# Performance work log

Hardware: AMD Instinct MI355X
Metric: run time of the kernel (lower is better)

The kernel has to match this reference:

```python
import jax, jax.numpy as jnp
import numpy as np

D = 512      # d_model
S = 8        # num_quantum_states
B, T = 16, 1024
LN_EPS = 1e-5


def setup_inputs() -> dict:
    key = jax.random.key(0)
    ks = jax.random.split(key, 10)
    sc = lambda fan_in: 1.0 / np.sqrt(fan_in)
    return {
        "x": jax.random.normal(ks[0], (B, T, D), dtype=jnp.float32),
        # entanglement gates: torch Linear weight [out=D, in=2D], bias [D], stacked over S
        "W_ent": jax.random.uniform(ks[1], (S, D, 2 * D), minval=-sc(2 * D), maxval=sc(2 * D)),
        "b_ent": jax.random.uniform(ks[2], (S, D), minval=-sc(2 * D), maxval=sc(2 * D)),
        # measurement MLP: Linear(D*S->D), LayerNorm(D), Tanh, Linear(D->1)
        "m1_w": jax.random.uniform(ks[3], (D, D * S), minval=-sc(D * S), maxval=sc(D * S)),
        "m1_b": jax.random.uniform(ks[4], (D,), minval=-sc(D * S), maxval=sc(D * S)),
        "ln_g": jnp.ones((D,), dtype=jnp.float32),
        "ln_b": jnp.zeros((D,), dtype=jnp.float32),
        "m2_w": jax.random.uniform(ks[5], (1, D), minval=-sc(D), maxval=sc(D)),
        "m2_b": jax.random.uniform(ks[6], (1,), minval=-sc(D), maxval=sc(D)),
    }


def _layernorm(h, g, b):
    mu = jnp.mean(h, axis=-1, keepdims=True)
    var = jnp.mean(jnp.square(h - mu), axis=-1, keepdims=True)
    return (h - mu) * jax.lax.rsqrt(var + LN_EPS) * g + b


def reference(x, W_ent, b_ent, m1_w, m1_b, ln_g, ln_b, m2_w, m2_b):
    b_, t_, d_ = x.shape
    s_ = W_ent.shape[0]
    # gate(cat[x_i, x_j]).mean(dim=2) == x_i @ W1^T + mean_j(x_j) @ W2^T + b  (exact algebra)
    W1 = W_ent[:, :, :d_]   # [S, D, D] acts on x_i
    W2 = W_ent[:, :, d_:]   # [S, D, D] acts on x_j (mean over j)
    xbar = jnp.mean(x, axis=1)                                   # [B, D]
    ent = (jnp.einsum('btd,sed->bste', x, W1)                    # [B, S, T, D]
           + jnp.einsum('bd,sed->bse', xbar, W2)[:, :, None, :]
           + b_ent[None, :, None, :])
    # permute(0,2,3,1).reshape(B,T,D*S): feature layout is (d, s) fastest on s
    qv = jnp.transpose(ent, (0, 2, 3, 1)).reshape(b_, t_, d_ * s_)
    h = jnp.tanh(_layernorm(qv @ m1_w.T + m1_b, ln_g, ln_b))     # [B, T, D]
    attn_logits = h @ m2_w.T + m2_b                              # [B, T, 1]
    attn_weights = jax.nn.softmax(attn_logits, axis=1)
    context = jnp.sum(attn_weights * x, axis=1)                  # [B, D]
    return context, attn_weights
```

## Files before the change

kernel.cpp:

```cpp
#include <hip/hip_runtime.h>
#include <hip/hip_bf16.h>

typedef __attribute__((ext_vector_type(8))) short bf16x8;
typedef __attribute__((ext_vector_type(4))) float f32x4;

__device__ __forceinline__ float bf2f(unsigned short u) {
    union { unsigned int i; float f; } c; c.i = ((unsigned int)u) << 16; return c.f;
}
__device__ __forceinline__ unsigned short f2bf(float f) {
    union { float f; unsigned int i; } c; c.f = f;
    unsigned int x = c.i;
    x += 0x7fffu + ((x >> 16) & 1u);
    return (unsigned short)(x >> 16);
}
__device__ __forceinline__ float tanh_fast(float v) {
    float a = fabsf(v);
    a = fminf(a, 15.0f);
    float e = __expf(2.0f * a);
    float t = 1.0f - 2.0f / (e + 1.0f);
    return copysignf(t, v);
}

#define GLOAD_LDS16(gp, lp) \
    __builtin_amdgcn_global_load_lds((const __attribute__((address_space(1))) void*)(gp), \
                                     (__attribute__((address_space(3))) void*)(lp), 16, 0, 0)

#define MFMA(a, b, c) __builtin_amdgcn_mfma_f32_16x16x32_bf16((a), (b), (c), 0, 0, 0)

#define SBAR()  __builtin_amdgcn_s_barrier()
#define SCHED0() __builtin_amdgcn_sched_barrier(0)


__global__ void k_sumx(const float* __restrict__ x, float* __restrict__ sumx) {
    int b = blockIdx.x, tc = blockIdx.y;
    int tid = threadIdx.x;
    const float* xp = x + ((size_t)b * 1024 + tc * 64) * 512;
    float a0 = 0.f, a1 = 0.f;
    for (int t = 0; t < 64; ++t) {
        a0 += xp[(size_t)t * 512 + tid];
        a1 += xp[(size_t)t * 512 + tid + 256];
    }
    atomicAdd(&sumx[b * 512 + tid], a0);
    atomicAdd(&sumx[b * 512 + tid + 256], a1);
}

__global__ void k_prepA(const float* __restrict__ m1w, const float* __restrict__ bent,
                        unsigned short* __restrict__ Abf, float* __restrict__ bias2) {
    int i = blockIdx.x, tid = threadIdx.x;
    const float* row = m1w + (size_t)i * 4096;
    float acc = 0.f;
    #pragma unroll
    for (int q = 0; q < 4; ++q) {
        int col = q * 1024 + tid * 4;
        float4 v = *(const float4*)(row + col);
        ushort4 o;
        o.x = f2bf(v.x); o.y = f2bf(v.y); o.z = f2bf(v.z); o.w = f2bf(v.w);
        *(ushort4*)(Abf + (size_t)i * 4096 + col) = o;
        int e0 = col >> 3, s0 = col & 7;
        acc += v.x * bent[(s0    ) * 512 + e0];
        acc += v.y * bent[(s0 + 1) * 512 + e0];
        acc += v.z * bent[(s0 + 2) * 512 + e0];
        acc += v.w * bent[(s0 + 3) * 512 + e0];
    }
    #pragma unroll
    for (int off = 32; off; off >>= 1) acc += __shfl_xor(acc, off);
    __shared__ float r4[4];
    if ((tid & 63) == 0) r4[tid >> 6] = acc;
    __syncthreads();
    if (tid == 0) bias2[i] = r4[0] + r4[1] + r4[2] + r4[3];
}

__global__ void k_conv_W(const float* __restrict__ W, unsigned short* __restrict__ WT) {
    __shared__ float tile[128][33];
    int e0 = blockIdx.x * 16;
    int j0 = blockIdx.y * 32;
    int tid = threadIdx.x;
    int tx = tid & 31, ty = tid >> 5;
    #pragma unroll
    for (int q = 0; q < 16; ++q) {
        int lk = q * 8 + ty;
        int de = lk >> 3, s = lk & 7;
        int r = s * 512 + e0 + de;
        tile[lk][tx] = W[(size_t)r * 1024 + j0 + tx];
    }
    __syncthreads();
    int j = tid >> 3, ck = (tid & 7) * 16;
    unsigned short* dst = WT + (size_t)(j0 + j) * 4096 + e0 * 8 + ck;
    #pragma unroll
    for (int g = 0; g < 4; ++g) {
        ushort4 o;
        o.x = f2bf(tile[ck + g * 4 + 0][j]);
        o.y = f2bf(tile[ck + g * 4 + 1][j]);
        o.z = f2bf(tile[ck + g * 4 + 2][j]);
        o.w = f2bf(tile[ck + g * 4 + 3][j]);
        *(ushort4*)(dst + g * 4) = o;
    }
}

__launch_bounds__(512, 2)
__global__ void k_gemm1(const unsigned short* __restrict__ Abf,
                        const unsigned short* __restrict__ WT,
                        float* __restrict__ CpL, float* __restrict__ CpR) {
    __shared__ __align__(16) unsigned short sA[2][64 * 64];
    __shared__ __align__(16) unsigned short sB[2][256 * 64];
    int i0 = blockIdx.x * 64;
    int j0 = blockIdx.y * 256;
    int kbase = blockIdx.z * 512;
    int tid = threadIdx.x, lane = tid & 63, w = tid >> 6;
    int wm = w >> 2, wn = w & 3;
    int lr = lane >> 3, sl = lane & 7;
    int lo = lane & 15, hi = lane >> 4;
    int arow = w * 8 + lr;
    const unsigned short* gA = Abf + (size_t)(i0 + arow) * 4096 + kbase + ((sl ^ lr) << 3);
    const unsigned short* gB0 = WT + (size_t)(j0 + w * 32 + 0 * 8 + lr) * 4096 + kbase + ((sl ^ lr) << 3);
    const unsigned short* gB1 = WT + (size_t)(j0 + w * 32 + 1 * 8 + lr) * 4096 + kbase + ((sl ^ lr) << 3);
    const unsigned short* gB2 = WT + (size_t)(j0 + w * 32 + 2 * 8 + lr) * 4096 + kbase + ((sl ^ lr) << 3);
    const unsigned short* gB3 = WT + (size_t)(j0 + w * 32 + 3 * 8 + lr) * 4096 + kbase + ((sl ^ lr) << 3);
    bool left = (blockIdx.y < 2);
    f32x4 acc[2][4] = {};

#define G1_STAGE(tt, bufn)                                                    \
    do {                                                                      \
        int koff = (tt) * 64;                                                 \
        GLOAD_LDS16(gA + koff, &sA[bufn][w * 8 * 64]);                        \
        GLOAD_LDS16(gB0 + koff, &sB[bufn][(w * 32 + 0) * 64]);                \
        GLOAD_LDS16(gB1 + koff, &sB[bufn][(w * 32 + 8) * 64]);                \
        GLOAD_LDS16(gB2 + koff, &sB[bufn][(w * 32 + 16) * 64]);               \
        GLOAD_LDS16(gB3 + koff, &sB[bufn][(w * 32 + 24) * 64]);               \
        SCHED0();                                                             \
    } while (0)

    G1_STAGE(0, 0);
    #pragma unroll
    for (int t = 0; t < 8; ++t) {
        int buf = t & 1;
        if (t < 7) {
            G1_STAGE(t + 1, buf ^ 1);
            asm volatile("s_waitcnt vmcnt(5)" ::: "memory");
        } else {
            asm volatile("s_waitcnt vmcnt(0)" ::: "memory");
        }
        SCHED0(); SBAR(); SCHED0();
        __builtin_amdgcn_s_setprio(1);
        #pragma unroll
        for (int kk = 0; kk < 2; ++kk) {
            int slotX = ((kk * 4 + hi) ^ (lo & 7)) << 3;
            bf16x8 a0 = *(const bf16x8*)(&sA[buf][(wm * 32 +      lo) * 64 + slotX]);
            bf16x8 a1 = *(const bf16x8*)(&sA[buf][(wm * 32 + 16 + lo) * 64 + slotX]);
            #pragma unroll
            for (int n = 0; n < 4; ++n) {
                bf16x8 bb = *(const bf16x8*)(&sB[buf][(wn * 64 + n * 16 + lo) * 64 + slotX]);
                if (left) {
                    acc[0][n] = MFMA(a0, bb, acc[0][n]);
                    acc[1][n] = MFMA(a1, bb, acc[1][n]);
                } else {
                    acc[0][n] = MFMA(bb, a0, acc[0][n]);
                    acc[1][n] = MFMA(bb, a1, acc[1][n]);
                }
            }
        }
        __builtin_amdgcn_s_setprio(0);
        if (t < 7) { SCHED0(); SBAR(); SCHED0(); }
    }
#undef G1_STAGE

    int ksoff = blockIdx.z * 262144;
    if (left) {
        #pragma unroll
        for (int m = 0; m < 2; ++m) {
            int ib = i0 + wm * 32 + m * 16 + hi * 4;
            #pragma unroll
            for (int n = 0; n < 4; ++n) {
                int j = j0 + wn * 64 + n * 16 + lo;
                #pragma unroll
                for (int r = 0; r < 4; ++r)
                    CpL[ksoff + (ib + r) * 512 + j] = acc[m][n][r];
            }
        }
    } else {
        #pragma unroll
        for (int m = 0; m < 2; ++m) {
            int ic = i0 + wm * 32 + m * 16 + lo;
            #pragma unroll
            for (int n = 0; n < 4; ++n) {
                int db = j0 - 512 + wn * 64 + n * 16 + hi * 4;
                #pragma unroll
                for (int r = 0; r < 4; ++r)
                    CpR[ksoff + (db + r) * 512 + ic] = acc[m][n][r];
            }
        }
    }
}

__global__ void k_reduce(const float* __restrict__ CpL, const float* __restrict__ CpR,
                         unsigned short* __restrict__ M1bf, unsigned short* __restrict__ M2t) {
    int bx = blockIdx.x;
    const float* Cp = (bx < 256) ? CpL : CpR;
    unsigned short* ob = (bx < 256) ? M1bf : M2t;
    int gid = (bx & 255) * 256 + threadIdx.x;
    float4 s = ((const float4*)Cp)[gid];
    #pragma unroll
    for (int ks = 1; ks < 8; ++ks) {
        float4 t = ((const float4*)Cp)[ks * 65536 + gid];
        s.x += t.x; s.y += t.y; s.z += t.z; s.w += t.w;
    }
    ushort4 o;
    o.x = f2bf(s.x); o.y = f2bf(s.y); o.z = f2bf(s.z); o.w = f2bf(s.w);
    ((ushort4*)ob)[gid] = o;
}

__global__ void k_cb(const float* __restrict__ sumx, const unsigned short* __restrict__ M2t,
                     const float* __restrict__ bias2, const float* __restrict__ m1b,
                     float* __restrict__ cbo) {
    int b = blockIdx.x, i0 = blockIdx.y * 64;
    int tid = threadIdx.x;
    int il = tid & 63, dq = tid >> 6;
    const float* sx = sumx + b * 512 + dq * 128;
    const unsigned short* mp = M2t + (size_t)dq * 128 * 512 + i0 + il;
    float acc = 0.f;
    #pragma unroll 4
    for (int dd = 0; dd < 128; ++dd)
        acc += sx[dd] * bf2f(mp[(size_t)dd * 512]);
    __shared__ float sPart[4][64];
    sPart[dq][il] = acc;
    __syncthreads();
    if (tid < 64) {
        float v = sPart[0][tid] + sPart[1][tid] + sPart[2][tid] + sPart[3][tid];
        cbo[b * 512 + i0 + tid] = v * (1.0f / 1024.0f) + bias2[i0 + tid] + m1b[i0 + tid];
    }
}

__launch_bounds__(512)
__global__ void k_gemm2(const float* __restrict__ x,
                        const unsigned short* __restrict__ M1bf,
                        const float* __restrict__ cb,
                        const float* __restrict__ lng, const float* __restrict__ lnb,
                        const float* __restrict__ m2w, const float* __restrict__ m2b,
                        float* __restrict__ logits) {
    __shared__ __align__(16) unsigned short sA[2][64 * 64];
    __shared__ __align__(16) unsigned short sB[2][512 * 64];
    __shared__ float sRed[2][8][64];
    __shared__ float sMu[64], sRs[64];
    __shared__ float sLp[8][64];
    int bt0 = blockIdx.x * 64;
    int b = bt0 >> 10;
    int tid = threadIdx.x, lane = tid & 63, w = tid >> 6;
    int wm = w >> 2, wn = w & 3;
    int lo = lane & 15, hi = lane >> 4;
    int lr = lane >> 3, sl = lane & 7;
    int arow = tid >> 3, aslot = tid & 7;
    const float* gA = x + (size_t)(bt0 + arow) * 512 + aslot * 8;
    int aoff = arow * 64 + ((aslot ^ (arow & 7)) << 3);
    const unsigned short* gB[8];
    #pragma unroll
    for (int g = 0; g < 8; ++g)
        gB[g] = M1bf + (size_t)(w * 64 + g * 8 + lr) * 512 + ((sl ^ lr) << 3);
    float4 pf0, pf1;
    f32x4 acc[2][8] = {};

#define G2_ISSUE(tt, bufn)                                                    \
    do {                                                                      \
        pf0 = *(const float4*)(gA + (tt) * 64);                               \
        pf1 = *(const float4*)(gA + (tt) * 64 + 4);                           \
        SCHED0();                                                             \
        _Pragma("unroll")                                                     \
        for (int g = 0; g < 8; ++g)                                           \
            GLOAD_LDS16(gB[g] + (tt) * 64, &sB[bufn][(w * 64 + g * 8) * 64]); \
        SCHED0();                                                             \
    } while (0)

#define G2_AWRITE(bufn)                                                      \
    do {                                                                     \
        bf16x8 pk;                                                           \
        pk[0] = (short)f2bf(pf0.x); pk[1] = (short)f2bf(pf0.y);              \
        pk[2] = (short)f2bf(pf0.z); pk[3] = (short)f2bf(pf0.w);              \
        pk[4] = (short)f2bf(pf1.x); pk[5] = (short)f2bf(pf1.y);              \
        pk[6] = (short)f2bf(pf1.z); pk[7] = (short)f2bf(pf1.w);              \
        *(bf16x8*)(&sA[bufn][aoff]) = pk;                                    \
    } while (0)

    G2_ISSUE(0, 0);
    asm volatile("s_waitcnt vmcnt(8)" ::: "memory");
    SCHED0();
    G2_AWRITE(0);
    asm volatile("s_waitcnt lgkmcnt(0)" ::: "memory");
    SCHED0();

    #pragma unroll
    for (int t = 0; t < 8; ++t) {
        int buf = t & 1;
        if (t < 7) {
            G2_ISSUE(t + 1, buf ^ 1);
            asm volatile("s_waitcnt vmcnt(10)" ::: "memory");
        } else {
            asm volatile("s_waitcnt vmcnt(0)" ::: "memory");
        }
        SCHED0(); SBAR(); SCHED0();
        __builtin_amdgcn_s_setprio(1);
        #pragma unroll
        for (int kk = 0; kk < 2; ++kk) {
            int slotX = ((kk * 4 + hi) ^ (lo & 7)) << 3;
            bf16x8 a0 = *(const bf16x8*)(&sA[buf][(wm * 32 +      lo) * 64 + slotX]);
            bf16x8 a1 = *(const bf16x8*)(&sA[buf][(wm * 32 + 16 + lo) * 64 + slotX]);
            #pragma unroll
            for (int n = 0; n < 8; ++n) {
                bf16x8 bb = *(const bf16x8*)(&sB[buf][(wn * 128 + n * 16 + lo) * 64 + slotX]);
                acc[0][n] = MFMA(a0, bb, acc[0][n]);
                acc[1][n] = MFMA(a1, bb, acc[1][n]);
            }
        }
        __builtin_amdgcn_s_setprio(0);
        if (t < 7) {
            asm volatile("s_waitcnt vmcnt(8)" ::: "memory");
            SCHED0();
            G2_AWRITE(buf ^ 1);
            asm volatile("s_waitcnt lgkmcnt(0)" ::: "memory");
            SCHED0(); SBAR(); SCHED0();
        }
    }
#undef G2_ISSUE
#undef G2_AWRITE

    #pragma unroll
    for (int n = 0; n < 8; ++n) {
        float cbv = cb[b * 512 + wn * 128 + n * 16 + lo];
        #pragma unroll
        for (int m = 0; m < 2; ++m)
            #pragma unroll
            for (int r = 0; r < 4; ++r)
                acc[m][n][r] += cbv;
    }
    #pragma unroll
    for (int m = 0; m < 2; ++m) {
        #pragma unroll
        for (int r = 0; r < 4; ++r) {
            float s1 = 0.f, s2 = 0.f;
            #pragma unroll
            for (int n = 0; n < 8; ++n) { float t = acc[m][n][r]; s1 += t; s2 += t * t; }
            #pragma unroll
            for (int msk = 1; msk < 16; msk <<= 1) {
                s1 += __shfl_xor(s1, msk);
                s2 += __shfl_xor(s2, msk);
            }
            if (lo == 0) {
                int row = wm * 32 + m * 16 + hi * 4 + r;
                sRed[0][w][row] = s1;
                sRed[1][w][row] = s2;
            }
        }
    }
    __syncthreads();
    if (tid < 64) {
        int wmr = tid >> 5;
        float s1 = 0.f, s2 = 0.f;
        #pragma unroll
        for (int q = 0; q < 4; ++q) { s1 += sRed[0][wmr * 4 + q][tid]; s2 += sRed[1][wmr * 4 + q][tid]; }
        float mu = s1 * (1.0f / 512.0f);
        float var = s2 * (1.0f / 512.0f) - mu * mu;
        sMu[tid] = mu;
        sRs[tid] = rsqrtf(var + 1e-5f);
    }
    __syncthreads();
    float gv[8], bv[8], wv[8];
    #pragma unroll
    for (int n = 0; n < 8; ++n) {
        int c = wn * 128 + n * 16 + lo;
        gv[n] = lng[c]; bv[n] = lnb[c]; wv[n] = m2w[c];
    }
    #pragma unroll
    for (int m = 0; m < 2; ++m) {
        #pragma unroll
        for (int r = 0; r < 4; ++r) {
            int row = wm * 32 + m * 16 + hi * 4 + r;
            float mu = sMu[row], rs = sRs[row];
            float lg = 0.f;
            #pragma unroll
            for (int n = 0; n < 8; ++n) {
                float h = tanh_fast((acc[m][n][r] - mu) * rs * gv[n] + bv[n]);
                lg += h * wv[n];
            }
            #pragma unroll
            for (int msk = 1; msk < 16; msk <<= 1) lg += __shfl_xor(lg, msk);
            if (lo == 0) sLp[w][row] = lg;
        }
    }
    __syncthreads();
    if (tid < 64) {
        int wmr = tid >> 5;
        float lg = 0.f;
        #pragma unroll
        for (int q = 0; q < 4; ++q) lg += sLp[wmr * 4 + q][tid];
        logits[bt0 + tid] = lg + m2b[0];
    }
}

__global__ void k_softmax(const float* __restrict__ logits, float* __restrict__ wout) {
    int b = blockIdx.x, tid = threadIdx.x;
    __shared__ float red[4];
    float4 v = ((const float4*)(logits + b * 1024))[tid];
    float mx = fmaxf(fmaxf(v.x, v.y), fmaxf(v.z, v.w));
    for (int off = 32; off; off >>= 1) mx = fmaxf(mx, __shfl_xor(mx, off));
    if ((tid & 63) == 0) red[tid >> 6] = mx;
    __syncthreads();
    mx = fmaxf(fmaxf(red[0], red[1]), fmaxf(red[2], red[3]));
    float e0 = expf(v.x - mx), e1 = expf(v.y - mx), e2 = expf(v.z - mx), e3 = expf(v.w - mx);
    float sm = e0 + e1 + e2 + e3;
    for (int off = 32; off; off >>= 1) sm += __shfl_xor(sm, off);
    __syncthreads();
    if ((tid & 63) == 0) red[tid >> 6] = sm;
    __syncthreads();
    float inv = 1.0f / (red[0] + red[1] + red[2] + red[3]);
    float4 o; o.x = e0 * inv; o.y = e1 * inv; o.z = e2 * inv; o.w = e3 * inv;
    ((float4*)(wout + b * 1024))[tid] = o;
}

__global__ void k_context(const float* __restrict__ x, const float* __restrict__ wts,
                          float* __restrict__ ctx) {
    int b = blockIdx.x, tc = blockIdx.y;
    int tid = threadIdx.x;
    const float* xp = x + ((size_t)b * 1024 + tc * 64) * 512;
    const float* wp = wts + b * 1024 + tc * 64;
    float a0 = 0.f, a1 = 0.f;
    for (int t = 0; t < 64; ++t) {
        float wv = wp[t];
        a0 += wv * xp[(size_t)t * 512 + tid];
        a1 += wv * xp[(size_t)t * 512 + tid + 256];
    }
    atomicAdd(&ctx[b * 512 + tid], a0);
    atomicAdd(&ctx[b * 512 + tid + 256], a1);
}

extern "C" void kernel_launch(void* const* d_in, const int* in_sizes, int n_in,
                              void* d_out, int out_size, void* d_ws, size_t ws_size,
                              hipStream_t stream) {
    (void)in_sizes; (void)n_in; (void)out_size; (void)ws_size;
    const float* x    = (const float*)d_in[0];
    const float* Went = (const float*)d_in[1];
    const float* bent = (const float*)d_in[2];
    const float* m1w  = (const float*)d_in[3];
    const float* m1b  = (const float*)d_in[4];
    const float* lng  = (const float*)d_in[5];
    const float* lnb  = (const float*)d_in[6];
    const float* m2w  = (const float*)d_in[7];
    const float* m2b  = (const float*)d_in[8];
    float* out = (float*)d_out;
    char* ws = (char*)d_ws;

    unsigned short* Abf   = (unsigned short*)(ws);
    unsigned short* WT    = (unsigned short*)(ws + 4194304);
    float* CpL            = (float*)(ws + 12582912);
    float* CpR            = (float*)(ws + 20971520);
    unsigned short* M1bf  = (unsigned short*)(ws + 29360128);
    unsigned short* M2t   = (unsigned short*)(ws + 29884416);
    float* sumx   = (float*)(ws + 30408704);
    float* bias2  = (float*)(ws + 30441472);
    float* cb     = (float*)(ws + 30443520);
    float* logits = (float*)(ws + 30476288);

    hipMemsetAsync(sumx, 0, 512 * 16 * sizeof(float), stream);
    hipMemsetAsync(out, 0, 8192 * sizeof(float), stream);

    k_sumx<<<dim3(16, 16), 256, 0, stream>>>(x, sumx);
    k_prepA<<<512, 256, 0, stream>>>(m1w, bent, Abf, bias2);
    k_conv_W<<<dim3(32, 32), 256, 0, stream>>>(Went, WT);
    k_gemm1<<<dim3(8, 4, 8), 512, 0, stream>>>(Abf, WT, CpL, CpR);
    k_reduce<<<512, 256, 0, stream>>>(CpL, CpR, M1bf, M2t);
    k_cb<<<dim3(16, 8), 256, 0, stream>>>(sumx, M2t, bias2, m1b, cb);
    k_gemm2<<<256, 512, 0, stream>>>(x, M1bf, cb, lng, lnb, m2w, m2b, logits);
    k_softmax<<<16, 256, 0, stream>>>(logits, out + 8192);
    k_context<<<dim3(16, 16), 256, 0, stream>>>(x, out + 8192, out);
}
```

Baseline: 90.34 us.

## Pre-swizzle M1 into MFMA fragment order and drop LDS staging in gemm2

The reduce kernel now writes the combined M1 matrix in a fragment-ordered layout, so gemm2 waves can load MFMA A operands straight from global memory with contiguous 16-byte reads. gemm2 no longer uses LDS double buffering or barriers in its main loop. It computes a transposed tile: each wave owns 64 output features across all 64 rows, with x converted to bf16 in registers via packed conversion. The goal is to remove LDS traffic and sync overhead, at the cost of every wave re-reading x from global/L2 and relying on caches for reuse of M1.

```diff
diff --git a/kernel.cpp b/kernel.cpp
--- a/kernel.cpp
+++ b/kernel.cpp
@@ -12,6 +12,10 @@
     unsigned int x = c.i;
     x += 0x7fffu + ((x >> 16) & 1u);
     return (unsigned short)(x >> 16);
+}
+__device__ __forceinline__ unsigned int pk2(float a, float b) {
+    __hip_bfloat162 h = __float22bfloat162_rn(float2{a, b});
+    union { __hip_bfloat162 h; unsigned int u; } c; c.h = h; return c.u;
 }
 __device__ __forceinline__ float tanh_fast(float v) {
     float a = fabsf(v);
@@ -193,10 +197,9 @@
 }
 
 __global__ void k_reduce(const float* __restrict__ CpL, const float* __restrict__ CpR,
-                         unsigned short* __restrict__ M1bf, unsigned short* __restrict__ M2t) {
+                         unsigned short* __restrict__ M1f, unsigned short* __restrict__ M2t) {
     int bx = blockIdx.x;
     const float* Cp = (bx < 256) ? CpL : CpR;
-    unsigned short* ob = (bx < 256) ? M1bf : M2t;
     int gid = (bx & 255) * 256 + threadIdx.x;
     float4 s = ((const float4*)Cp)[gid];
     #pragma unroll
@@ -206,7 +209,14 @@
     }
     ushort4 o;
     o.x = f2bf(s.x); o.y = f2bf(s.y); o.z = f2bf(s.z); o.w = f2bf(s.w);
-    ((ushort4*)ob)[gid] = o;
+    if (bx < 256) {
+        int i = gid >> 7, k = (gid & 127) << 2;
+        size_t off = ((size_t)((i >> 4) * 16 + (k >> 5)) << 9)
+                   + (((k >> 3) & 3) << 7) + ((i & 15) << 3) + (k & 7);
+        *(ushort4*)(M1f + off) = o;
+    } else {
+        ((ushort4*)M2t)[gid] = o;
+    }
 }
 
 __global__ void k_cb(const float* __restrict__ sumx, const unsigned short* __restrict__ M2t,
@@ -232,165 +242,128 @@
 
 __launch_bounds__(512)
 __global__ void k_gemm2(const float* __restrict__ x,
-                        const unsigned short* __restrict__ M1bf,
+                        const unsigned short* __restrict__ M1f,
                         const float* __restrict__ cb,
                         const float* __restrict__ lng, const float* __restrict__ lnb,
                         const float* __restrict__ m2w, const float* __restrict__ m2b,
                         float* __restrict__ logits) {
-    __shared__ __align__(16) unsigned short sA[2][64 * 64];
-    __shared__ __align__(16) unsigned short sB[2][512 * 64];
-    __shared__ float sRed[2][8][64];
+    __shared__ float sStat[8][2][64];
     __shared__ float sMu[64], sRs[64];
     __shared__ float sLp[8][64];
     int bt0 = blockIdx.x * 64;
     int b = bt0 >> 10;
     int tid = threadIdx.x, lane = tid & 63, w = tid >> 6;
-    int wm = w >> 2, wn = w & 3;
     int lo = lane & 15, hi = lane >> 4;
-    int lr = lane >> 3, sl = lane & 7;
-    int arow = tid >> 3, aslot = tid & 7;
-    const float* gA = x + (size_t)(bt0 + arow) * 512 + aslot * 8;
-    int aoff = arow * 64 + ((aslot ^ (arow & 7)) << 3);
-    const unsigned short* gB[8];
-    #pragma unroll
-    for (int g = 0; g < 8; ++g)
-        gB[g] = M1bf + (size_t)(w * 64 + g * 8 + lr) * 512 + ((sl ^ lr) << 3);
-    float4 pf0, pf1;
-    f32x4 acc[2][8] = {};
-
-#define G2_ISSUE(tt, bufn)                                                    \
-    do {                                                                      \
-        pf0 = *(const float4*)(gA + (tt) * 64);                               \
-        pf1 = *(const float4*)(gA + (tt) * 64 + 4);                           \
-        SCHED0();                                                             \
-        _Pragma("unroll")                                                     \
-        for (int g = 0; g < 8; ++g)                                           \
-            GLOAD_LDS16(gB[g] + (tt) * 64, &sB[bufn][(w * 64 + g * 8) * 64]); \
-        SCHED0();                                                             \
-    } while (0)
-
-#define G2_AWRITE(bufn)                                                      \
-    do {                                                                     \
-        bf16x8 pk;                                                           \
-        pk[0] = (short)f2bf(pf0.x); pk[1] = (short)f2bf(pf0.y);              \
-        pk[2] = (short)f2bf(pf0.z); pk[3] = (short)f2bf(pf0.w);              \
-        pk[4] = (short)f2bf(pf1.x); pk[5] = (short)f2bf(pf1.y);              \
-        pk[6] = (short)f2bf(pf1.z); pk[7] = (short)f2bf(pf1.w);              \
-        *(bf16x8*)(&sA[bufn][aoff]) = pk;                                    \
-    } while (0)
-
-    G2_ISSUE(0, 0);
-    asm volatile("s_waitcnt vmcnt(8)" ::: "memory");
-    SCHED0();
-    G2_AWRITE(0);
-    asm volatile("s_waitcnt lgkmcnt(0)" ::: "memory");
-    SCHED0();
-
-    #pragma unroll
-    for (int t = 0; t < 8; ++t) {
-        int buf = t & 1;
-        if (t < 7) {
-            G2_ISSUE(t + 1, buf ^ 1);
-            asm volatile("s_waitcnt vmcnt(10)" ::: "memory");
-        } else {
-            asm volatile("s_waitcnt vmcnt(0)" ::: "memory");
-        }
-        SCHED0(); SBAR(); SCHED0();
-        __builtin_amdgcn_s_setprio(1);
-        #pragma unroll
-        for (int kk = 0; kk < 2; ++kk) {
-            int slotX = ((kk * 4 + hi) ^ (lo & 7)) << 3;
-            bf16x8 a0 = *(const bf16x8*)(&sA[buf][(wm * 32 +      lo) * 64 + slotX]);
-            bf16x8 a1 = *(const bf16x8*)(&sA[buf][(wm * 32 + 16 + lo) * 64 + slotX]);
+    const unsigned short* aP = M1f + ((size_t)(w * 4 * 16) << 9) + lane * 8;
+    const float* xr0 = x + (size_t)(bt0 +  0 + lo) * 512 + hi * 8;
+    const float* xr1 = x + (size_t)(bt0 + 16 + lo) * 512 + hi * 8;
+    const float* xr2 = x + (size_t)(bt0 + 32 + lo) * 512 + hi * 8;
+    const float* xr3 = x + (size_t)(bt0 + 48 + lo) * 512 + hi * 8;
+    f32x4 acc[4][4] = {};
+    #pragma unroll 4
+    for (int fk = 0; fk < 16; ++fk) {
+        bf16x8 av[4], bv[4];
+        #pragma unroll
+        for (int m = 0; m < 4; ++m)
+            av[m] = *(const bf16x8*)(aP + ((m * 16 + fk) << 9));
+        {
+            float4 f0, f1;
+            union { unsigned int u[4]; bf16x8 v; } pk;
+            f0 = *(const float4*)(xr0 + fk * 32); f1 = *(const float4*)(xr0 + fk * 32 + 4);
+            pk.u[0] = pk2(f0.x, f0.y); pk.u[1] = pk2(f0.z, f0.w);
+            pk.u[2] = pk2(f1.x, f1.y); pk.u[3] = pk2(f1.z, f1.w);
+            bv[0] = pk.v;
+            f0 = *(const float4*)(xr1 + fk * 32); f1 = *(const float4*)(xr1 + fk * 32 + 4);
+            pk.u[0] = pk2(f0.x, f0.y); pk.u[1] = pk2(f0.z, f0.w);
+            pk.u[2] = pk2(f1.x, f1.y); pk.u[3] = pk2(f1.z, f1.w);
+            bv[1] = pk.v;
+            f0 = *(const float4*)(xr2 + fk * 32); f1 = *(const float4*)(xr2 + fk * 32 + 4);
+            pk.u[0] = pk2(f0.x, f0.y); pk.u[1] = pk2(f0.z, f0.w);
+            pk.u[2] = pk2(f1.x, f1.y); pk.u[3] = pk2(f1.z, f1.w);
+            bv[2] = pk.v;
+            f0 = *(const float4*)(xr3 + fk * 32); f1 = *(const float4*)(xr3 + fk * 32 + 4);
+            pk.u[0] = pk2(f0.x, f0.y); pk.u[1] = pk2(f0.z, f0.w);
+            pk.u[2] = pk2(f1.x, f1.y); pk.u[3] = pk2(f1.z, f1.w);
+            bv[3] = pk.v;
+        }
+        #pragma unroll
+        for (int m = 0; m < 4; ++m)
             #pragma unroll
-            for (int n = 0; n < 8; ++n) {
-                bf16x8 bb = *(const bf16x8*)(&sB[buf][(wn * 128 + n * 16 + lo) * 64 + slotX]);
-                acc[0][n] = MFMA(a0, bb, acc[0][n]);
-                acc[1][n] = MFMA(a1, bb, acc[1][n]);
-            }
-        }
-        __builtin_amdgcn_s_setprio(0);
-        if (t < 7) {
-            asm volatile("s_waitcnt vmcnt(8)" ::: "memory");
-            SCHED0();
-            G2_AWRITE(buf ^ 1);
-            asm volatile("s_waitcnt lgkmcnt(0)" ::: "memory");
-            SCHED0(); SBAR(); SCHED0();
-        }
-    }
-#undef G2_ISSUE
-#undef G2_AWRITE
-
-    #pragma unroll
-    for (int n = 0; n < 8; ++n) {
-        float cbv = cb[b * 512 + wn * 128 + n * 16 + lo];
-        #pragma unroll
-        for (int m = 0; m < 2; ++m)
+            for (int n = 0; n < 4; ++n)
+                acc[m][n] = MFMA(av[m], bv[n], acc[m][n]);
+    }
+    #pragma unroll
+    for (int m = 0; m < 4; ++m) {
+        float4 c4 = *(const float4*)(cb + b * 512 + w * 64 + m * 16 + hi * 4);
+        #pragma unroll
+        for (int n = 0; n < 4; ++n) {
+            acc[m][n][0] += c4.x; acc[m][n][1] += c4.y;
+            acc[m][n][2] += c4.z; acc[m][n][3] += c4.w;
+        }
+    }
+    float s1[4], s2[4];
+    #pragma unroll
+    for (int n = 0; n < 4; ++n) {
+        float a1 = 0.f, a2 = 0.f;
+        #pragma unroll
+        for (int m = 0; m < 4; ++m)
             #pragma unroll
-            for (int r = 0; r < 4; ++r)
-                acc[m][n][r] += cbv;
-    }
-    #pragma unroll
-    for (int m = 0; m < 2; ++m) {
-        #pragma unroll
-        for (int r = 0; r < 4; ++r) {
-            float s1 = 0.f, s2 = 0.f;
-            #pragma unroll
-            for (int n = 0; n < 8; ++n) { float t = acc[m][n][r]; s1 += t; s2 += t * t; }
-            #pragma unroll
-            for (int msk = 1; msk < 16; msk <<= 1) {
-                s1 += __shfl_xor(s1, msk);
-                s2 += __shfl_xor(s2, msk);
-            }
-            if (lo == 0) {
-                int row = wm * 32 + m * 16 + hi * 4 + r;
-                sRed[0][w][row] = s1;
-                sRed[1][w][row] = s2;
-            }
+            for (int r = 0; r < 4; ++r) { float t = acc[m][n][r]; a1 += t; a2 += t * t; }
+        a1 += __shfl_xor(a1, 16); a1 += __shfl_xor(a1, 32);
+        a2 += __shfl_xor(a2, 16); a2 += __shfl_xor(a2, 32);
+        s1[n] = a1; s2[n] = a2;
+    }
+    if (lane < 16) {
+        #pragma unroll
+        for (int n = 0; n < 4; ++n) {
+            sStat[w][0][n * 16 + lane] = s1[n];
+            sStat[w][1][n * 16 + lane] = s2[n];
         }
     }
     __syncthreads();
     if (tid < 64) {
-        int wmr = tid >> 5;
-        float s1 = 0.f, s2 = 0.f;
-        #pragma unroll
-        for (int q = 0; q < 4; ++q) { s1 += sRed[0][wmr * 4 + q][tid]; s2 += sRed[1][wmr * 4 + q][tid]; }
-        float mu = s1 * (1.0f / 512.0f);
-        float var = s2 * (1.0f / 512.0f) - mu * mu;
+        float a1 = 0.f, a2 = 0.f;
+        #pragma unroll
+        for (int ww = 0; ww < 8; ++ww) { a1 += sStat[ww][0][tid]; a2 += sStat[ww][1][tid]; }
+        float mu = a1 * (1.0f / 512.0f);
+        float var = a2 * (1.0f / 512.0f) - mu * mu;
         sMu[tid] = mu;
         sRs[tid] = rsqrtf(var + 1e-5f);
     }
     __syncthreads();
-    float gv[8], bv[8], wv[8];
-    #pragma unroll
-    for (int n = 0; n < 8; ++n) {
-        int c = wn * 128 + n * 16 + lo;
-        gv[n] = lng[c]; bv[n] = lnb[c]; wv[n] = m2w[c];
-    }
-    #pragma unroll
-    for (int m = 0; m < 2; ++m) {
-        #pragma unroll
-        for (int r = 0; r < 4; ++r) {
-            int row = wm * 32 + m * 16 + hi * 4 + r;
-            float mu = sMu[row], rs = sRs[row];
-            float lg = 0.f;
-            #pragma unroll
-            for (int n = 0; n < 8; ++n) {
-                float h = tanh_fast((acc[m][n][r] - mu) * rs * gv[n] + bv[n]);
-                lg += h * wv[n];
-            }
-            #pragma unroll
-            for (int msk = 1; msk < 16; msk <<= 1) lg += __shfl_xor(lg, msk);
-            if (lo == 0) sLp[w][row] = lg;
-        }
+    float4 g4[4], b4[4], w4[4];
+    #pragma unroll
+    for (int m = 0; m < 4; ++m) {
+        int ib = w * 64 + m * 16 + hi * 4;
+        g4[m] = *(const float4*)(lng + ib);
+        b4[m] = *(const float4*)(lnb + ib);
+        w4[m] = *(const float4*)(m2w + ib);
+    }
+    float lg[4];
+    #pragma unroll
+    for (int n = 0; n < 4; ++n) {
+        float mu = sMu[n * 16 + lo], rs = sRs[n * 16 + lo];
+        float a = 0.f;
+        #pragma unroll
+        for (int m = 0; m < 4; ++m) {
+            a += tanh_fast((acc[m][n][0] - mu) * rs * g4[m].x + b4[m].x) * w4[m].x;
+            a += tanh_fast((acc[m][n][1] - mu) * rs * g4[m].y + b4[m].y) * w4[m].y;
+            a += tanh_fast((acc[m][n][2] - mu) * rs * g4[m].z + b4[m].z) * w4[m].z;
+            a += tanh_fast((acc[m][n][3] - mu) * rs * g4[m].w + b4[m].w) * w4[m].w;
+        }
+        a += __shfl_xor(a, 16); a += __shfl_xor(a, 32);
+        lg[n] = a;
+    }
+    if (lane < 16) {
+        #pragma unroll
+        for (int n = 0; n < 4; ++n) sLp[w][n * 16 + lane] = lg[n];
     }
     __syncthreads();
     if (tid < 64) {
-        int wmr = tid >> 5;
-        float lg = 0.f;
-        #pragma unroll
-        for (int q = 0; q < 4; ++q) lg += sLp[wmr * 4 + q][tid];
-        logits[bt0 + tid] = lg + m2b[0];
+        float t = 0.f;
+        #pragma unroll
+        for (int ww = 0; ww < 8; ++ww) t += sLp[ww][tid];
+        logits[bt0 + tid] = t + m2b[0];
     }
 }
 
@@ -450,7 +423,7 @@
     unsigned short* WT    = (unsigned short*)(ws + 4194304);
     float* CpL            = (float*)(ws + 12582912);
     float* CpR            = (float*)(ws + 20971520);
-    unsigned short* M1bf  = (unsigned short*)(ws + 29360128);
+    unsigned short* M1f   = (unsigned short*)(ws + 29360128);
     unsigned short* M2t   = (unsigned short*)(ws + 29884416);
     float* sumx   = (float*)(ws + 30408704);
     float* bias2  = (float*)(ws + 30441472);
@@ -464,9 +437,9 @@
     k_prepA<<<512, 256, 0, stream>>>(m1w, bent, Abf, bias2);
     k_conv_W<<<dim3(32, 32), 256, 0, stream>>>(Went, WT);
     k_gemm1<<<dim3(8, 4, 8), 512, 0, stream>>>(Abf, WT, CpL, CpR);
-    k_reduce<<<512, 256, 0, stream>>>(CpL, CpR, M1bf, M2t);
+    k_reduce<<<512, 256, 0, stream>>>(CpL, CpR, M1f, M2t);
     k_cb<<<dim3(16, 8), 256, 0, stream>>>(sumx, M2t, bias2, m1b, cb);
-    k_gemm2<<<256, 512, 0, stream>>>(x, M1bf, cb, lng, lnb, m2w, m2b, logits);
+    k_gemm2<<<256, 512, 0, stream>>>(x, M1f, cb, lng, lnb, m2w, m2b, logits);
     k_softmax<<<16, 256, 0, stream>>>(logits, out + 8192);
     k_context<<<dim3(16, 16), 256, 0, stream>>>(x, out + 8192, out);
 }
```

New measurement: 112.8 us. +24.9%, slower.

## Split gemm2 into plain GEMM with bf16 output and separate LayerNorm-logit kernel

Applied to the files above, without the earlier changes.

The fused GEMM+LayerNorm+tanh+logit kernel is split in two. The first kernel does only the x·M1 GEMM, now single-buffered with __syncthreads instead of the hand-scheduled double-buffered pipeline, and stores its accumulators as packed bf16 to workspace reusing the CpL region. A second kernel reloads each 64-row tile into LDS, adds the cb bias, and computes the LayerNorm statistics, tanh and dot with m2w. This likely aims to shorten the GEMM's register-heavy epilogue and raise occupancy. The cost is an extra launch, a 16 MB bf16 round trip through memory, extra bf16 rounding before LayerNorm, and loss of load/compute overlap in the GEMM loop.

```diff
diff --git a/kernel.cpp b/kernel.cpp
--- a/kernel.cpp
+++ b/kernel.cpp
@@ -12,6 +12,10 @@
     unsigned int x = c.i;
     x += 0x7fffu + ((x >> 16) & 1u);
     return (unsigned short)(x >> 16);
+}
+__device__ __forceinline__ unsigned int pk2(float a, float b) {
+    __hip_bfloat162 h = __float22bfloat162_rn(float2{a, b});
+    union { __hip_bfloat162 h; unsigned int u; } c; c.h = h; return c.u;
 }
 __device__ __forceinline__ float tanh_fast(float v) {
     float a = fabsf(v);
@@ -231,166 +235,140 @@
 }
 
 __launch_bounds__(512)
-__global__ void k_gemm2(const float* __restrict__ x,
-                        const unsigned short* __restrict__ M1bf,
-                        const float* __restrict__ cb,
-                        const float* __restrict__ lng, const float* __restrict__ lnb,
-                        const float* __restrict__ m2w, const float* __restrict__ m2b,
-                        float* __restrict__ logits) {
-    __shared__ __align__(16) unsigned short sA[2][64 * 64];
-    __shared__ __align__(16) unsigned short sB[2][512 * 64];
-    __shared__ float sRed[2][8][64];
-    __shared__ float sMu[64], sRs[64];
-    __shared__ float sLp[8][64];
+__global__ void k_gemm2s(const float* __restrict__ x,
+                         const unsigned short* __restrict__ M1bf,
+                         unsigned short* __restrict__ ypk) {
+    __shared__ __align__(16) unsigned short sA[64 * 64];
+    __shared__ __align__(16) unsigned short sB[512 * 64];
     int bt0 = blockIdx.x * 64;
-    int b = bt0 >> 10;
     int tid = threadIdx.x, lane = tid & 63, w = tid >> 6;
     int wm = w >> 2, wn = w & 3;
     int lo = lane & 15, hi = lane >> 4;
     int lr = lane >> 3, sl = lane & 7;
     int arow = tid >> 3, aslot = tid & 7;
     const float* gA = x + (size_t)(bt0 + arow) * 512 + aslot * 8;
-    int aoff = arow * 64 + ((aslot ^ (arow & 7)) << 3);
+    unsigned short* dAp = sA + arow * 64 + ((aslot ^ (arow & 7)) << 3);
     const unsigned short* gB[8];
     #pragma unroll
     for (int g = 0; g < 8; ++g)
         gB[g] = M1bf + (size_t)(w * 64 + g * 8 + lr) * 512 + ((sl ^ lr) << 3);
-    float4 pf0, pf1;
     f32x4 acc[2][8] = {};
-
-#define G2_ISSUE(tt, bufn)                                                    \
-    do {                                                                      \
-        pf0 = *(const float4*)(gA + (tt) * 64);                               \
-        pf1 = *(const float4*)(gA + (tt) * 64 + 4);                           \
-        SCHED0();                                                             \
-        _Pragma("unroll")                                                     \
-        for (int g = 0; g < 8; ++g)                                           \
-            GLOAD_LDS16(gB[g] + (tt) * 64, &sB[bufn][(w * 64 + g * 8) * 64]); \
-        SCHED0();                                                             \
-    } while (0)
-
-#define G2_AWRITE(bufn)                                                      \
-    do {                                                                     \
-        bf16x8 pk;                                                           \
-        pk[0] = (short)f2bf(pf0.x); pk[1] = (short)f2bf(pf0.y);              \
-        pk[2] = (short)f2bf(pf0.z); pk[3] = (short)f2bf(pf0.w);              \
-        pk[4] = (short)f2bf(pf1.x); pk[5] = (short)f2bf(pf1.y);              \
-        pk[6] = (short)f2bf(pf1.z); pk[7] = (short)f2bf(pf1.w);              \
-        *(bf16x8*)(&sA[bufn][aoff]) = pk;                                    \
-    } while (0)
-
-    G2_ISSUE(0, 0);
-    asm volatile("s_waitcnt vmcnt(8)" ::: "memory");
-    SCHED0();
-    G2_AWRITE(0);
-    asm volatile("s_waitcnt lgkmcnt(0)" ::: "memory");
-    SCHED0();
-
-    #pragma unroll
-    for (int t = 0; t < 8; ++t) {
-        int buf = t & 1;
-        if (t < 7) {
-            G2_ISSUE(t + 1, buf ^ 1);
-            asm volatile("s_waitcnt vmcnt(10)" ::: "memory");
-        } else {
-            asm volatile("s_waitcnt vmcnt(0)" ::: "memory");
-        }
-        SCHED0(); SBAR(); SCHED0();
-        __builtin_amdgcn_s_setprio(1);
+    for (int k0 = 0; k0 < 512; k0 += 64) {
+        if (k0) __syncthreads();
+        #pragma unroll
+        for (int g = 0; g < 8; ++g)
+            GLOAD_LDS16(gB[g] + k0, &sB[(w * 64 + g * 8) * 64]);
+        float4 f0 = *(const float4*)(gA + k0);
+        float4 f1 = *(const float4*)(gA + k0 + 4);
+        bf16x8 pk;
+        pk[0] = (short)f2bf(f0.x); pk[1] = (short)f2bf(f0.y);
+        pk[2] = (short)f2bf(f0.z); pk[3] = (short)f2bf(f0.w);
+        pk[4] = (short)f2bf(f1.x); pk[5] = (short)f2bf(f1.y);
+        pk[6] = (short)f2bf(f1.z); pk[7] = (short)f2bf(f1.w);
+        *(bf16x8*)dAp = pk;
+        __syncthreads();
         #pragma unroll
         for (int kk = 0; kk < 2; ++kk) {
             int slotX = ((kk * 4 + hi) ^ (lo & 7)) << 3;
-            bf16x8 a0 = *(const bf16x8*)(&sA[buf][(wm * 32 +      lo) * 64 + slotX]);
-            bf16x8 a1 = *(const bf16x8*)(&sA[buf][(wm * 32 + 16 + lo) * 64 + slotX]);
+            bf16x8 a0 = *(const bf16x8*)(sA + (wm * 32 +      lo) * 64 + slotX);
+            bf16x8 a1 = *(const bf16x8*)(sA + (wm * 32 + 16 + lo) * 64 + slotX);
             #pragma unroll
             for (int n = 0; n < 8; ++n) {
-                bf16x8 bb = *(const bf16x8*)(&sB[buf][(wn * 128 + n * 16 + lo) * 64 + slotX]);
+                bf16x8 bb = *(const bf16x8*)(sB + (wn * 128 + n * 16 + lo) * 64 + slotX);
                 acc[0][n] = MFMA(a0, bb, acc[0][n]);
                 acc[1][n] = MFMA(a1, bb, acc[1][n]);
             }
         }
-        __builtin_amdgcn_s_setprio(0);
-        if (t < 7) {
-            asm volatile("s_waitcnt vmcnt(8)" ::: "memory");
-            SCHED0();
-            G2_AWRITE(buf ^ 1);
-            asm volatile("s_waitcnt lgkmcnt(0)" ::: "memory");
-            SCHED0(); SBAR(); SCHED0();
-        }
-    }
-#undef G2_ISSUE
-#undef G2_AWRITE
-
-    #pragma unroll
-    for (int n = 0; n < 8; ++n) {
-        float cbv = cb[b * 512 + wn * 128 + n * 16 + lo];
-        #pragma unroll
-        for (int m = 0; m < 2; ++m)
-            #pragma unroll
-            for (int r = 0; r < 4; ++r)
-                acc[m][n][r] += cbv;
-    }
+    }
+    unsigned short* yb = ypk + (size_t)blockIdx.x * 32768;
     #pragma unroll
     for (int m = 0; m < 2; ++m) {
         #pragma unroll
-        for (int r = 0; r < 4; ++r) {
-            float s1 = 0.f, s2 = 0.f;
-            #pragma unroll
-            for (int n = 0; n < 8; ++n) { float t = acc[m][n][r]; s1 += t; s2 += t * t; }
-            #pragma unroll
-            for (int msk = 1; msk < 16; msk <<= 1) {
-                s1 += __shfl_xor(s1, msk);
-                s2 += __shfl_xor(s2, msk);
-            }
-            if (lo == 0) {
-                int row = wm * 32 + m * 16 + hi * 4 + r;
-                sRed[0][w][row] = s1;
-                sRed[1][w][row] = s2;
-            }
-        }
-    }
-    __syncthreads();
-    if (tid < 64) {
-        int wmr = tid >> 5;
-        float s1 = 0.f, s2 = 0.f;
-        #pragma unroll
-        for (int q = 0; q < 4; ++q) { s1 += sRed[0][wmr * 4 + q][tid]; s2 += sRed[1][wmr * 4 + q][tid]; }
-        float mu = s1 * (1.0f / 512.0f);
-        float var = s2 * (1.0f / 512.0f) - mu * mu;
-        sMu[tid] = mu;
-        sRs[tid] = rsqrtf(var + 1e-5f);
-    }
-    __syncthreads();
-    float gv[8], bv[8], wv[8];
-    #pragma unroll
-    for (int n = 0; n < 8; ++n) {
-        int c = wn * 128 + n * 16 + lo;
-        gv[n] = lng[c]; bv[n] = lnb[c]; wv[n] = m2w[c];
-    }
-    #pragma unroll
-    for (int m = 0; m < 2; ++m) {
-        #pragma unroll
-        for (int r = 0; r < 4; ++r) {
-            int row = wm * 32 + m * 16 + hi * 4 + r;
-            float mu = sMu[row], rs = sRs[row];
-            float lg = 0.f;
-            #pragma unroll
-            for (int n = 0; n < 8; ++n) {
-                float h = tanh_fast((acc[m][n][r] - mu) * rs * gv[n] + bv[n]);
-                lg += h * wv[n];
-            }
-            #pragma unroll
-            for (int msk = 1; msk < 16; msk <<= 1) lg += __shfl_xor(lg, msk);
-            if (lo == 0) sLp[w][row] = lg;
-        }
-    }
-    __syncthreads();
-    if (tid < 64) {
-        int wmr = tid >> 5;
-        float lg = 0.f;
-        #pragma unroll
-        for (int q = 0; q < 4; ++q) lg += sLp[wmr * 4 + q][tid];
-        logits[bt0 + tid] = lg + m2b[0];
+        for (int n = 0; n < 8; ++n) {
+            unsigned int u0 = pk2(acc[m][n][0], acc[m][n][1]);
+            unsigned int u1 = pk2(acc[m][n][2], acc[m][n][3]);
+            uint2 o; o.x = u0; o.y = u1;
+            *(uint2*)(yb + (((w * 16 + m * 8 + n) << 8) + (lane << 2))) = o;
+        }
+    }
+}
+
+__launch_bounds__(512)
+__global__ void k_lnlogit(const unsigned short* __restrict__ ypk,
+                          const float* __restrict__ cb,
+                          const float* __restrict__ lng, const float* __restrict__ lnb,
+                          const float* __restrict__ m2w, const float* __restrict__ m2b,
+                          float* __restrict__ logits) {
+    __shared__ __align__(16) unsigned short sY[32768];
+    __shared__ float sCb[512], sG[512], sBe[512], sW[512];
+    __shared__ float sS1[64][8], sS2[64][8], sLg[64][8];
+    int blk = blockIdx.x;
+    int bt0 = blk * 64;
+    int b = bt0 >> 10;
+    int tid = threadIdx.x, w = tid >> 6, lane = tid & 63;
+    sCb[tid] = cb[b * 512 + tid];
+    sG[tid]  = lng[tid];
+    sBe[tid] = lnb[tid];
+    sW[tid]  = m2w[tid];
+    const unsigned short* src = ypk + (size_t)blk * 32768;
+    #pragma unroll
+    for (int it = 0; it < 8; ++it) {
+        int off = (w * 8 + it) * 512;
+        GLOAD_LDS16(src + off + (lane << 3), &sY[off]);
+    }
+    asm volatile("s_waitcnt vmcnt(0)" ::: "memory");
+    __syncthreads();
+
+    int row = tid >> 3, sub = tid & 7;
+    int wm = row >> 5, m = (row >> 4) & 1, hi = (row >> 2) & 3, r = row & 3;
+    float s1 = 0.f, s2 = 0.f;
+    #pragma unroll
+    for (int wn = 0; wn < 4; ++wn) {
+        #pragma unroll
+        for (int n = 0; n < 8; ++n) {
+            int c = (wm * 4 + wn) * 16 + m * 8 + n;
+            int eb = c * 256 + r;
+            int ib = wn * 128 + n * 16;
+            #pragma unroll
+            for (int l2 = 0; l2 < 2; ++l2) {
+                int lo = sub * 2 + l2;
+                float v = bf2f(sY[eb + (hi * 16 + lo) * 4]) + sCb[ib + lo];
+                s1 += v; s2 += v * v;
+            }
+        }
+    }
+    sS1[row][sub] = s1; sS2[row][sub] = s2;
+    __syncthreads();
+    float a1 = 0.f, a2 = 0.f;
+    #pragma unroll
+    for (int q = 0; q < 8; ++q) { a1 += sS1[row][q]; a2 += sS2[row][q]; }
+    float mu = a1 * (1.0f / 512.0f);
+    float var = a2 * (1.0f / 512.0f) - mu * mu;
+    float rs = rsqrtf(var + 1e-5f);
+    float lg = 0.f;
+    #pragma unroll
+    for (int wn = 0; wn < 4; ++wn) {
+        #pragma unroll
+        for (int n = 0; n < 8; ++n) {
+            int c = (wm * 4 + wn) * 16 + m * 8 + n;
+            int eb = c * 256 + r;
+            int ib = wn * 128 + n * 16;
+            #pragma unroll
+            for (int l2 = 0; l2 < 2; ++l2) {
+                int lo = sub * 2 + l2;
+                float v = bf2f(sY[eb + (hi * 16 + lo) * 4]) + sCb[ib + lo];
+                float h = tanh_fast((v - mu) * rs * sG[ib + lo] + sBe[ib + lo]);
+                lg += h * sW[ib + lo];
+            }
+        }
+    }
+    sLg[row][sub] = lg;
+    __syncthreads();
+    if (sub == 0) {
+        float t = 0.f;
+        #pragma unroll
+        for (int q = 0; q < 8; ++q) t += sLg[row][q];
+        logits[bt0 + row] = t + m2b[0];
     }
 }
 
@@ -450,6 +428,7 @@
     unsigned short* WT    = (unsigned short*)(ws + 4194304);
     float* CpL            = (float*)(ws + 12582912);
     float* CpR            = (float*)(ws + 20971520);
+    unsigned short* ypk   = (unsigned short*)(ws + 12582912);
     unsigned short* M1bf  = (unsigned short*)(ws + 29360128);
     unsigned short* M2t   = (unsigned short*)(ws + 29884416);
     float* sumx   = (float*)(ws + 30408704);
@@ -466,7 +445,8 @@
     k_gemm1<<<dim3(8, 4, 8), 512, 0, stream>>>(Abf, WT, CpL, CpR);
     k_reduce<<<512, 256, 0, stream>>>(CpL, CpR, M1bf, M2t);
     k_cb<<<dim3(16, 8), 256, 0, stream>>>(sumx, M2t, bias2, m1b, cb);
-    k_gemm2<<<256, 512, 0, stream>>>(x, M1bf, cb, lng, lnb, m2w, m2b, logits);
+    k_gemm2s<<<256, 512, 0, stream>>>(x, M1bf, ypk);
+    k_lnlogit<<<256, 512, 0, stream>>>(ypk, cb, lng, lnb, m2w, m2b, logits);
     k_softmax<<<16, 256, 0, stream>>>(logits, out + 8192);
     k_context<<<dim3(16, 16), 256, 0, stream>>>(x, out + 8192, out);
 }
```

After: 98.89 us. 1.09x slower.
